# Optimization experiments

Hardware: AMD Instinct MI355X
Metric: run time of the kernel (lower is better)

## Reference

```python
import jax, jax.numpy as jnp
import numpy as np

TOP_K = 2
EPS = 1e-6


def setup_inputs() -> dict:
    key = jax.random.key(0)
    ks = jax.random.split(key, 8)
    B, S, D, E = 4, 2048, 2048, 8
    sd = 1.0 / np.sqrt(D)
    return {
        "x": jax.random.normal(ks[0], (B, S, D), dtype=jnp.float32),
        "Wr": jax.random.normal(ks[1], (D, E), dtype=jnp.float32) * sd,
        "br": jnp.zeros((E,), dtype=jnp.float32),
        "We": jax.random.normal(ks[2], (E, D, D), dtype=jnp.float32) * sd,
        "be": jnp.zeros((E, D), dtype=jnp.float32),
        "Wo": jax.random.normal(ks[3], (D, D), dtype=jnp.float32) * sd,
        "bo": jnp.zeros((D,), dtype=jnp.float32),
        "norm_w": jnp.ones((D,), dtype=jnp.float32),
    }


def reference(x, Wr, br, We, be, Wo, bo, norm_w):
    B, S, D = x.shape
    xf = x.reshape(-1, D)  # [T, D]
    # Router + top-k gating (softmax over the k selected logits, as in source)
    logits = xf @ Wr + br                      # [T, E]
    vals, idx = jax.lax.top_k(logits, TOP_K)   # [T, K]
    gates = jax.nn.softmax(vals, axis=-1)      # [T, K]
    # Expert FFN: Linear -> SiLU (dropout=0 -> identity). Dense over all experts,
    # then gather the top-k outputs per token.
    all_out = jax.nn.silu(jnp.einsum('td,edf->tef', xf, We) + be)  # [T, E, D]
    picked = jnp.take_along_axis(all_out, idx[:, :, None], axis=1)  # [T, K, D]
    combined = jnp.sum(gates[:, :, None] * picked, axis=1)          # [T, D]
    out = combined @ Wo + bo
    y = xf + out
    rms = jnp.sqrt(jnp.mean(y * y, axis=-1, keepdims=True) + EPS)
    return (norm_w * (y / rms)).reshape(B, S, D)
```

## Files before the change

kernel.cpp:

```cpp
#include <hip/hip_runtime.h>
#include <hip/hip_bf16.h>
#include <stdint.h>

typedef __bf16 bf16;
typedef __bf16 bf16x4 __attribute__((ext_vector_type(4)));
typedef __bf16 bf16x8 __attribute__((ext_vector_type(8)));
typedef float floatx4 __attribute__((ext_vector_type(4)));

#define T_TOK 8192
#define DIM 2048
#define NE 8

__device__ inline void gld_lds16(const bf16* g, bf16* l) {
  __builtin_amdgcn_global_load_lds(
      (const __attribute__((address_space(1))) uint32_t*)g,
      (__attribute__((address_space(3))) uint32_t*)l, 16, 0, 0);
}

__global__ __launch_bounds__(256) void transpose_convert(
    const float* __restrict__ in, bf16* __restrict__ out) {
  __shared__ float tile[32][33];
  const int tx = threadIdx.x & 31;
  const int ty = threadIdx.x >> 5;
  const int n0 = blockIdx.x * 32;
  const int k0 = blockIdx.y * 32;
  const size_t base = (size_t)blockIdx.z * DIM * DIM;
  const float* src = in + base;
  bf16* dst = out + base;
#pragma unroll
  for (int i = 0; i < 32; i += 8)
    tile[ty + i][tx] = src[(size_t)(k0 + ty + i) * DIM + n0 + tx];
  __syncthreads();
#pragma unroll
  for (int i = 0; i < 32; i += 8)
    dst[(size_t)(n0 + ty + i) * DIM + k0 + tx] = (bf16)tile[tx][ty + i];
}

__global__ __launch_bounds__(256) void router_kernel(
    const float* __restrict__ x, const float* __restrict__ Wr,
    const float* __restrict__ br, int* __restrict__ cnt,
    int* __restrict__ aid_list, float* __restrict__ gate_list,
    bf16* __restrict__ xb) {
  const int t = blockIdx.x;
  const int tid = threadIdx.x;
  const float* xr = x + (size_t)t * DIM;
  bf16* xbr = xb + (size_t)t * DIM;
  float acc[8];
#pragma unroll
  for (int e = 0; e < 8; ++e) acc[e] = 0.f;
#pragma unroll
  for (int h = 0; h < 2; ++h) {
    const int d0 = tid * 4 + h * 1024;
    float4 xv = *(const float4*)&xr[d0];
    bf16x4 xc;
    xc[0] = (bf16)xv.x; xc[1] = (bf16)xv.y; xc[2] = (bf16)xv.z; xc[3] = (bf16)xv.w;
    *(bf16x4*)&xbr[d0] = xc;
    const float* wp = &Wr[(size_t)d0 * NE];
    float xe[4] = {xv.x, xv.y, xv.z, xv.w};
#pragma unroll
    for (int q = 0; q < 4; ++q) {
      float4 w0 = *(const float4*)&wp[q * 8];
      float4 w1 = *(const float4*)&wp[q * 8 + 4];
      acc[0] += xe[q] * w0.x; acc[1] += xe[q] * w0.y;
      acc[2] += xe[q] * w0.z; acc[3] += xe[q] * w0.w;
      acc[4] += xe[q] * w1.x; acc[5] += xe[q] * w1.y;
      acc[6] += xe[q] * w1.z; acc[7] += xe[q] * w1.w;
    }
  }
#pragma unroll
  for (int e = 0; e < 8; ++e) {
#pragma unroll
    for (int off = 32; off > 0; off >>= 1) acc[e] += __shfl_down(acc[e], off, 64);
  }
  __shared__ float red[4][8];
  const int lane = tid & 63, wid = tid >> 6;
  if (lane == 0) {
#pragma unroll
    for (int e = 0; e < 8; ++e) red[wid][e] = acc[e];
  }
  __syncthreads();
  if (tid == 0) {
    float lg[8];
#pragma unroll
    for (int e = 0; e < 8; ++e)
      lg[e] = red[0][e] + red[1][e] + red[2][e] + red[3][e] + br[e];
    int i0 = 0;
#pragma unroll
    for (int e = 1; e < 8; ++e) if (lg[e] > lg[i0]) i0 = e;
    int i1 = (i0 == 0) ? 1 : 0;
#pragma unroll
    for (int e = 0; e < 8; ++e)
      if (e != i0 && lg[e] > lg[i1]) i1 = e;
    const float g0 = 1.f / (1.f + expf(lg[i1] - lg[i0]));
    const float g1 = 1.f - g0;
    int p0 = atomicAdd(&cnt[i0], 1);
    aid_list[i0 * T_TOK + p0] = t * 2;
    gate_list[i0 * T_TOK + p0] = g0;
    int p1 = atomicAdd(&cnt[i1], 1);
    aid_list[i1 * T_TOK + p1] = t * 2 + 1;
    gate_list[i1 * T_TOK + p1] = g1;
  }
}

__global__ __launch_bounds__(256, 2) void expert_gemm(
    const bf16* __restrict__ xb, const bf16* __restrict__ Wt,
    const float* __restrict__ be, const int* __restrict__ cnt,
    const int* __restrict__ aid_list, const float* __restrict__ gate_list,
    bf16* __restrict__ aout) {
  const int e = blockIdx.z;
  const int ne = cnt[e];
  const int m0 = blockIdx.x * 128;
  if (m0 >= ne) return;
  const int n0 = blockIdx.y * 128;
  const int tid = threadIdx.x;

  __shared__ bf16 As[128][32];
  __shared__ bf16 Bs[128][32];
  __shared__ int aidS[128];
  __shared__ float gateS[128];

  if (tid < 128) {
    const int idx = m0 + tid;
    aidS[tid] = (idx < ne) ? aid_list[e * T_TOK + idx] : 0;
    gateS[tid] = (idx < ne) ? gate_list[e * T_TOK + idx] : 0.f;
  }
  __syncthreads();

  const int kq = (tid & 3) * 8;
  const int row0 = tid >> 2;
  const int row1 = 64 + (tid >> 2);
  const bf16* ap0 = xb + (size_t)(aidS[row0] >> 1) * DIM + kq;
  const bf16* ap1 = xb + (size_t)(aidS[row1] >> 1) * DIM + kq;
  const bf16* wbase = Wt + (size_t)e * DIM * DIM;
  const bf16* bp0 = wbase + (size_t)(n0 + row0) * DIM + kq;
  const bf16* bp1 = wbase + (size_t)(n0 + row1) * DIM + kq;
  bf16* asd0 = &As[0][0] + (size_t)tid * 8;
  bf16* asd1 = &As[0][0] + ((size_t)tid + 256) * 8;
  bf16* bsd0 = &Bs[0][0] + (size_t)tid * 8;
  bf16* bsd1 = &Bs[0][0] + ((size_t)tid + 256) * 8;

  const int lane = tid & 63, wid = tid >> 6;
  const int wr = (wid >> 1) * 64, wc = (wid & 1) * 64;
  const int quad = lane >> 4, l15 = lane & 15;

  floatx4 acc[4][4];
#pragma unroll
  for (int i = 0; i < 4; ++i)
#pragma unroll
    for (int j = 0; j < 4; ++j) acc[i][j] = (floatx4){0.f, 0.f, 0.f, 0.f};

  for (int k0 = 0; k0 < DIM; k0 += 32) {
    gld_lds16(bp0 + k0, bsd0);
    gld_lds16(bp1 + k0, bsd1);
    gld_lds16(ap0 + k0, asd0);
    gld_lds16(ap1 + k0, asd1);
    __syncthreads();

    bf16x8 af[4], bfr[4];
#pragma unroll
    for (int i = 0; i < 4; ++i)
      af[i] = *(const bf16x8*)&As[wr + i * 16 + l15][quad * 8];
#pragma unroll
    for (int j = 0; j < 4; ++j)
      bfr[j] = *(const bf16x8*)&Bs[wc + j * 16 + l15][quad * 8];
#pragma unroll
    for (int i = 0; i < 4; ++i)
#pragma unroll
      for (int j = 0; j < 4; ++j)
        acc[i][j] = __builtin_amdgcn_mfma_f32_16x16x32_bf16(af[i], bfr[j], acc[i][j], 0, 0, 0);
    __syncthreads();
  }

#pragma unroll
  for (int j = 0; j < 4; ++j) {
    const int col = n0 + wc + j * 16 + l15;
    const float bev = be[e * DIM + col];
#pragma unroll
    for (int i = 0; i < 4; ++i) {
#pragma unroll
      for (int r = 0; r < 4; ++r) {
        const int rl = wr + i * 16 + quad * 4 + r;
        if (m0 + rl < ne) {
          float v = acc[i][j][r] + bev;
          v = v / (1.f + __expf(-v));
          v *= gateS[rl];
          aout[(size_t)aidS[rl] * DIM + col] = (bf16)v;
        }
      }
    }
  }
}

__global__ __launch_bounds__(256) void combine_kernel(
    const bf16* __restrict__ aout, bf16* __restrict__ hcomb) {
  const size_t i = ((size_t)blockIdx.x * 256 + threadIdx.x) * 8;
  const size_t row = i >> 11;
  const size_t d = i & 2047;
  const bf16* a0 = aout + (row << 12) + d;
  bf16x8 u0 = *(const bf16x8*)a0;
  bf16x8 u1 = *(const bf16x8*)(a0 + DIM);
  bf16x8 s;
#pragma unroll
  for (int q = 0; q < 8; ++q) s[q] = (bf16)((float)u0[q] + (float)u1[q]);
  *(bf16x8*)&hcomb[i] = s;
}

__global__ __launch_bounds__(256, 2) void proj_gemm(
    const bf16* __restrict__ hcomb, const bf16* __restrict__ Wot,
    const float* __restrict__ bo, const float* __restrict__ x,
    float* __restrict__ y) {
  const int m0 = blockIdx.x * 128;
  const int n0 = blockIdx.y * 128;
  const int tid = threadIdx.x;

  __shared__ bf16 As[128][32];
  __shared__ bf16 Bs[128][32];

  const int kq = (tid & 3) * 8;
  const int row0 = tid >> 2;
  const int row1 = 64 + (tid >> 2);
  const bf16* ap0 = hcomb + (size_t)(m0 + row0) * DIM + kq;
  const bf16* ap1 = hcomb + (size_t)(m0 + row1) * DIM + kq;
  const bf16* bp0 = Wot + (size_t)(n0 + row0) * DIM + kq;
  const bf16* bp1 = Wot + (size_t)(n0 + row1) * DIM + kq;
  bf16* asd0 = &As[0][0] + (size_t)tid * 8;
  bf16* asd1 = &As[0][0] + ((size_t)tid + 256) * 8;
  bf16* bsd0 = &Bs[0][0] + (size_t)tid * 8;
  bf16* bsd1 = &Bs[0][0] + ((size_t)tid + 256) * 8;

  const int lane = tid & 63, wid = tid >> 6;
  const int wr = (wid >> 1) * 64, wc = (wid & 1) * 64;
  const int quad = lane >> 4, l15 = lane & 15;

  floatx4 acc[4][4];
#pragma unroll
  for (int i = 0; i < 4; ++i)
#pragma unroll
    for (int j = 0; j < 4; ++j) acc[i][j] = (floatx4){0.f, 0.f, 0.f, 0.f};

  for (int k0 = 0; k0 < DIM; k0 += 32) {
    gld_lds16(bp0 + k0, bsd0);
    gld_lds16(bp1 + k0, bsd1);
    gld_lds16(ap0 + k0, asd0);
    gld_lds16(ap1 + k0, asd1);
    __syncthreads();

    bf16x8 af[4], bfr[4];
#pragma unroll
    for (int i = 0; i < 4; ++i)
      af[i] = *(const bf16x8*)&As[wr + i * 16 + l15][quad * 8];
#pragma unroll
    for (int j = 0; j < 4; ++j)
      bfr[j] = *(const bf16x8*)&Bs[wc + j * 16 + l15][quad * 8];
#pragma unroll
    for (int i = 0; i < 4; ++i)
#pragma unroll
      for (int j = 0; j < 4; ++j)
        acc[i][j] = __builtin_amdgcn_mfma_f32_16x16x32_bf16(af[i], bfr[j], acc[i][j], 0, 0, 0);
    __syncthreads();
  }

#pragma unroll
  for (int j = 0; j < 4; ++j) {
    const int col = n0 + wc + j * 16 + l15;
    const float bov = bo[col];
#pragma unroll
    for (int i = 0; i < 4; ++i) {
#pragma unroll
      for (int r = 0; r < 4; ++r) {
        const int rl = wr + i * 16 + quad * 4 + r;
        const size_t o = (size_t)(m0 + rl) * DIM + col;
        y[o] = acc[i][j][r] + bov + x[o];
      }
    }
  }
}

__global__ __launch_bounds__(256) void rmsnorm_kernel(
    float* __restrict__ y, const float* __restrict__ w) {
  const int row = blockIdx.x;
  const int tid = threadIdx.x;
  float* yr = y + (size_t)row * DIM;
  float4 v0 = ((const float4*)yr)[tid];
  float4 v1 = ((const float4*)yr)[tid + 256];
  float ss = v0.x * v0.x + v0.y * v0.y + v0.z * v0.z + v0.w * v0.w +
             v1.x * v1.x + v1.y * v1.y + v1.z * v1.z + v1.w * v1.w;
#pragma unroll
  for (int off = 32; off > 0; off >>= 1) ss += __shfl_down(ss, off, 64);
  __shared__ float s4[4];
  const int lane = tid & 63, wid = tid >> 6;
  if (lane == 0) s4[wid] = ss;
  __syncthreads();
  const float tot = s4[0] + s4[1] + s4[2] + s4[3];
  const float r = rsqrtf(tot / (float)DIM + 1e-6f);
  float4 w0 = ((const float4*)w)[tid];
  float4 w1 = ((const float4*)w)[tid + 256];
  float4 o0 = make_float4(v0.x * r * w0.x, v0.y * r * w0.y, v0.z * r * w0.z, v0.w * r * w0.w);
  float4 o1 = make_float4(v1.x * r * w1.x, v1.y * r * w1.y, v1.z * r * w1.z, v1.w * r * w1.w);
  ((float4*)yr)[tid] = o0;
  ((float4*)yr)[tid + 256] = o1;
}

extern "C" void kernel_launch(void* const* d_in, const int* in_sizes, int n_in,
                              void* d_out, int out_size, void* d_ws, size_t ws_size,
                              hipStream_t stream) {
  const float* x  = (const float*)d_in[0];
  const float* Wr = (const float*)d_in[1];
  const float* br = (const float*)d_in[2];
  const float* We = (const float*)d_in[3];
  const float* be = (const float*)d_in[4];
  const float* Wo = (const float*)d_in[5];
  const float* bo = (const float*)d_in[6];
  const float* nw = (const float*)d_in[7];
  float* out = (float*)d_out;

  uint8_t* ws = (uint8_t*)d_ws;
  size_t off = 0;
  auto carve = [&](size_t bytes) -> void* {
    void* p = ws + off;
    off += (bytes + 255) & ~(size_t)255;
    return p;
  };
  int*   cnt       = (int*)carve(NE * sizeof(int));
  int*   aid_list  = (int*)carve((size_t)NE * T_TOK * sizeof(int));
  float* gate_list = (float*)carve((size_t)NE * T_TOK * sizeof(float));
  bf16*  We_t      = (bf16*)carve((size_t)NE * DIM * DIM * sizeof(bf16));
  bf16*  Wo_t      = (bf16*)carve((size_t)DIM * DIM * sizeof(bf16));
  bf16*  aoutb     = (bf16*)carve((size_t)T_TOK * 2 * DIM * sizeof(bf16));
  bf16*  xb        = (bf16*)carve((size_t)T_TOK * DIM * sizeof(bf16));
  bf16*  hcomb     = We_t;
  (void)ws_size; (void)in_sizes; (void)n_in; (void)out_size;

  hipMemsetAsync(cnt, 0, NE * sizeof(int), stream);
  transpose_convert<<<dim3(DIM / 32, DIM / 32, NE), 256, 0, stream>>>(We, We_t);
  transpose_convert<<<dim3(DIM / 32, DIM / 32, 1), 256, 0, stream>>>(Wo, Wo_t);
  router_kernel<<<T_TOK, 256, 0, stream>>>(x, Wr, br, cnt, aid_list, gate_list, xb);
  expert_gemm<<<dim3(T_TOK / 128, DIM / 128, NE), 256, 0, stream>>>(
      xb, We_t, be, cnt, aid_list, gate_list, aoutb);
  combine_kernel<<<(T_TOK * DIM / 8) / 256, 256, 0, stream>>>(aoutb, hcomb);
  proj_gemm<<<dim3(T_TOK / 128, DIM / 128), 256, 0, stream>>>(hcomb, Wo_t, bo, x, out);
  rmsnorm_kernel<<<T_TOK, 256, 0, stream>>>(out, nw);
}
```

Before: 952.8 us.

## Compact expert tile grid and widen GEMM K-tile to 64 with XOR-swizzled LDS

A new single-thread kernel builds a compact list of (expert, row-offset) chunks, so expert_gemm launches only blocks that have work instead of a sparse 64x8 grid where most blocks exit early. Both the expert and projection GEMMs now load 64-wide K tiles per barrier pair, halving the number of synchronizations. An XOR swizzle on the LDS layout is meant to avoid bank conflicts on fragment reads. The cost is an extra tiny serial launch, double the LDS per block (which may lower occupancy), and a fixed MAX_CHUNKS bound.

```diff
diff --git a/kernel.cpp b/kernel.cpp
--- a/kernel.cpp
+++ b/kernel.cpp
@@ -10,6 +10,7 @@
 #define T_TOK 8192
 #define DIM 2048
 #define NE 8
+#define MAX_CHUNKS 136
 
 __device__ inline void gld_lds16(const bf16* g, bf16* l) {
   __builtin_amdgcn_global_load_lds(
@@ -102,20 +103,37 @@
   }
 }
 
+__global__ void build_chunks(const int* __restrict__ cnt, int2* __restrict__ chunks,
+                             int* __restrict__ nchunks) {
+  if (threadIdx.x == 0 && blockIdx.x == 0) {
+    int tot = 0;
+#pragma unroll
+    for (int e = 0; e < NE; ++e) {
+      const int ne = cnt[e];
+      for (int m0 = 0; m0 < ne; m0 += 128) chunks[tot++] = make_int2(e, m0);
+    }
+    *nchunks = tot;
+  }
+}
+
+
 __global__ __launch_bounds__(256, 2) void expert_gemm(
     const bf16* __restrict__ xb, const bf16* __restrict__ Wt,
     const float* __restrict__ be, const int* __restrict__ cnt,
     const int* __restrict__ aid_list, const float* __restrict__ gate_list,
+    const int2* __restrict__ chunks, const int* __restrict__ nchunks,
     bf16* __restrict__ aout) {
-  const int e = blockIdx.z;
+  const int cid = blockIdx.x;
+  if (cid >= *nchunks) return;
+  const int2 ch = chunks[cid];
+  const int e = ch.x;
+  const int m0 = ch.y;
   const int ne = cnt[e];
-  const int m0 = blockIdx.x * 128;
-  if (m0 >= ne) return;
   const int n0 = blockIdx.y * 128;
   const int tid = threadIdx.x;
 
-  __shared__ bf16 As[128][32];
-  __shared__ bf16 Bs[128][32];
+  __shared__ bf16 As[128][64];
+  __shared__ bf16 Bs[128][64];
   __shared__ int aidS[128];
   __shared__ float gateS[128];
 
@@ -126,18 +144,19 @@
   }
   __syncthreads();
 
-  const int kq = (tid & 3) * 8;
-  const int row0 = tid >> 2;
-  const int row1 = 64 + (tid >> 2);
-  const bf16* ap0 = xb + (size_t)(aidS[row0] >> 1) * DIM + kq;
-  const bf16* ap1 = xb + (size_t)(aidS[row1] >> 1) * DIM + kq;
+  const int r0 = tid >> 3;
+  const int kq = (((tid & 7) ^ (r0 & 7))) * 8;
   const bf16* wbase = Wt + (size_t)e * DIM * DIM;
-  const bf16* bp0 = wbase + (size_t)(n0 + row0) * DIM + kq;
-  const bf16* bp1 = wbase + (size_t)(n0 + row1) * DIM + kq;
-  bf16* asd0 = &As[0][0] + (size_t)tid * 8;
-  bf16* asd1 = &As[0][0] + ((size_t)tid + 256) * 8;
-  bf16* bsd0 = &Bs[0][0] + (size_t)tid * 8;
-  bf16* bsd1 = &Bs[0][0] + ((size_t)tid + 256) * 8;
+  const bf16* ap[4];
+  const bf16* bp[4];
+#pragma unroll
+  for (int h = 0; h < 4; ++h) {
+    const int r = r0 + 32 * h;
+    ap[h] = xb + (size_t)(aidS[r] >> 1) * DIM + kq;
+    bp[h] = wbase + (size_t)(n0 + r) * DIM + kq;
+  }
+  bf16* const asF = &As[0][0];
+  bf16* const bsF = &Bs[0][0];
 
   const int lane = tid & 63, wid = tid >> 6;
   const int wr = (wid >> 1) * 64, wc = (wid & 1) * 64;
@@ -149,25 +168,40 @@
 #pragma unroll
     for (int j = 0; j < 4; ++j) acc[i][j] = (floatx4){0.f, 0.f, 0.f, 0.f};
 
-  for (int k0 = 0; k0 < DIM; k0 += 32) {
-    gld_lds16(bp0 + k0, bsd0);
-    gld_lds16(bp1 + k0, bsd1);
-    gld_lds16(ap0 + k0, asd0);
-    gld_lds16(ap1 + k0, asd1);
+  int aoff[2][4], boff[2][4];
+#pragma unroll
+  for (int s = 0; s < 2; ++s) {
+    const int kb = s * 4 + quad;
+#pragma unroll
+    for (int i = 0; i < 4; ++i) {
+      const int mi = wr + i * 16 + l15;
+      aoff[s][i] = mi * 64 + ((kb ^ (mi & 7)) * 8);
+      const int nj = wc + i * 16 + l15;
+      boff[s][i] = nj * 64 + ((kb ^ (nj & 7)) * 8);
+    }
+  }
+
+  for (int k0 = 0; k0 < DIM; k0 += 64) {
+#pragma unroll
+    for (int h = 0; h < 4; ++h) {
+      gld_lds16(bp[h] + k0, bsF + ((size_t)tid + 256 * h) * 8);
+      gld_lds16(ap[h] + k0, asF + ((size_t)tid + 256 * h) * 8);
+    }
     __syncthreads();
 
-    bf16x8 af[4], bfr[4];
-#pragma unroll
-    for (int i = 0; i < 4; ++i)
-      af[i] = *(const bf16x8*)&As[wr + i * 16 + l15][quad * 8];
-#pragma unroll
-    for (int j = 0; j < 4; ++j)
-      bfr[j] = *(const bf16x8*)&Bs[wc + j * 16 + l15][quad * 8];
-#pragma unroll
-    for (int i = 0; i < 4; ++i)
-#pragma unroll
-      for (int j = 0; j < 4; ++j)
-        acc[i][j] = __builtin_amdgcn_mfma_f32_16x16x32_bf16(af[i], bfr[j], acc[i][j], 0, 0, 0);
+#pragma unroll
+    for (int s = 0; s < 2; ++s) {
+      bf16x8 af[4], bfr[4];
+#pragma unroll
+      for (int i = 0; i < 4; ++i) af[i] = *(const bf16x8*)&asF[aoff[s][i]];
+#pragma unroll
+      for (int j = 0; j < 4; ++j) bfr[j] = *(const bf16x8*)&bsF[boff[s][j]];
+#pragma unroll
+      for (int i = 0; i < 4; ++i)
+#pragma unroll
+        for (int j = 0; j < 4; ++j)
+          acc[i][j] = __builtin_amdgcn_mfma_f32_16x16x32_bf16(af[i], bfr[j], acc[i][j], 0, 0, 0);
+    }
     __syncthreads();
   }
 
@@ -213,20 +247,21 @@
   const int n0 = blockIdx.y * 128;
   const int tid = threadIdx.x;
 
-  __shared__ bf16 As[128][32];
-  __shared__ bf16 Bs[128][32];
-
-  const int kq = (tid & 3) * 8;
-  const int row0 = tid >> 2;
-  const int row1 = 64 + (tid >> 2);
-  const bf16* ap0 = hcomb + (size_t)(m0 + row0) * DIM + kq;
-  const bf16* ap1 = hcomb + (size_t)(m0 + row1) * DIM + kq;
-  const bf16* bp0 = Wot + (size_t)(n0 + row0) * DIM + kq;
-  const bf16* bp1 = Wot + (size_t)(n0 + row1) * DIM + kq;
-  bf16* asd0 = &As[0][0] + (size_t)tid * 8;
-  bf16* asd1 = &As[0][0] + ((size_t)tid + 256) * 8;
-  bf16* bsd0 = &Bs[0][0] + (size_t)tid * 8;
-  bf16* bsd1 = &Bs[0][0] + ((size_t)tid + 256) * 8;
+  __shared__ bf16 As[128][64];
+  __shared__ bf16 Bs[128][64];
+
+  const int r0 = tid >> 3;
+  const int kq = (((tid & 7) ^ (r0 & 7))) * 8;
+  const bf16* ap[4];
+  const bf16* bp[4];
+#pragma unroll
+  for (int h = 0; h < 4; ++h) {
+    const int r = r0 + 32 * h;
+    ap[h] = hcomb + (size_t)(m0 + r) * DIM + kq;
+    bp[h] = Wot + (size_t)(n0 + r) * DIM + kq;
+  }
+  bf16* const asF = &As[0][0];
+  bf16* const bsF = &Bs[0][0];
 
   const int lane = tid & 63, wid = tid >> 6;
   const int wr = (wid >> 1) * 64, wc = (wid & 1) * 64;
@@ -238,25 +273,40 @@
 #pragma unroll
     for (int j = 0; j < 4; ++j) acc[i][j] = (floatx4){0.f, 0.f, 0.f, 0.f};
 
-  for (int k0 = 0; k0 < DIM; k0 += 32) {
-    gld_lds16(bp0 + k0, bsd0);
-    gld_lds16(bp1 + k0, bsd1);
-    gld_lds16(ap0 + k0, asd0);
-    gld_lds16(ap1 + k0, asd1);
+  int aoff[2][4], boff[2][4];
+#pragma unroll
+  for (int s = 0; s < 2; ++s) {
+    const int kb = s * 4 + quad;
+#pragma unroll
+    for (int i = 0; i < 4; ++i) {
+      const int mi = wr + i * 16 + l15;
+      aoff[s][i] = mi * 64 + ((kb ^ (mi & 7)) * 8);
+      const int nj = wc + i * 16 + l15;
+      boff[s][i] = nj * 64 + ((kb ^ (nj & 7)) * 8);
+    }
+  }
+
+  for (int k0 = 0; k0 < DIM; k0 += 64) {
+#pragma unroll
+    for (int h = 0; h < 4; ++h) {
+      gld_lds16(bp[h] + k0, bsF + ((size_t)tid + 256 * h) * 8);
+      gld_lds16(ap[h] + k0, asF + ((size_t)tid + 256 * h) * 8);
+    }
     __syncthreads();
 
-    bf16x8 af[4], bfr[4];
-#pragma unroll
-    for (int i = 0; i < 4; ++i)
-      af[i] = *(const bf16x8*)&As[wr + i * 16 + l15][quad * 8];
-#pragma unroll
-    for (int j = 0; j < 4; ++j)
-      bfr[j] = *(const bf16x8*)&Bs[wc + j * 16 + l15][quad * 8];
-#pragma unroll
-    for (int i = 0; i < 4; ++i)
-#pragma unroll
-      for (int j = 0; j < 4; ++j)
-        acc[i][j] = __builtin_amdgcn_mfma_f32_16x16x32_bf16(af[i], bfr[j], acc[i][j], 0, 0, 0);
+#pragma unroll
+    for (int s = 0; s < 2; ++s) {
+      bf16x8 af[4], bfr[4];
+#pragma unroll
+      for (int i = 0; i < 4; ++i) af[i] = *(const bf16x8*)&asF[aoff[s][i]];
+#pragma unroll
+      for (int j = 0; j < 4; ++j) bfr[j] = *(const bf16x8*)&bsF[boff[s][j]];
+#pragma unroll
+      for (int i = 0; i < 4; ++i)
+#pragma unroll
+        for (int j = 0; j < 4; ++j)
+          acc[i][j] = __builtin_amdgcn_mfma_f32_16x16x32_bf16(af[i], bfr[j], acc[i][j], 0, 0, 0);
+    }
     __syncthreads();
   }
 
@@ -324,6 +374,8 @@
   int*   cnt       = (int*)carve(NE * sizeof(int));
   int*   aid_list  = (int*)carve((size_t)NE * T_TOK * sizeof(int));
   float* gate_list = (float*)carve((size_t)NE * T_TOK * sizeof(float));
+  int2*  chunks    = (int2*)carve(MAX_CHUNKS * sizeof(int2));
+  int*   nchunks   = (int*)carve(sizeof(int));
   bf16*  We_t      = (bf16*)carve((size_t)NE * DIM * DIM * sizeof(bf16));
   bf16*  Wo_t      = (bf16*)carve((size_t)DIM * DIM * sizeof(bf16));
   bf16*  aoutb     = (bf16*)carve((size_t)T_TOK * 2 * DIM * sizeof(bf16));
@@ -335,8 +387,9 @@
   transpose_convert<<<dim3(DIM / 32, DIM / 32, NE), 256, 0, stream>>>(We, We_t);
   transpose_convert<<<dim3(DIM / 32, DIM / 32, 1), 256, 0, stream>>>(Wo, Wo_t);
   router_kernel<<<T_TOK, 256, 0, stream>>>(x, Wr, br, cnt, aid_list, gate_list, xb);
-  expert_gemm<<<dim3(T_TOK / 128, DIM / 128, NE), 256, 0, stream>>>(
-      xb, We_t, be, cnt, aid_list, gate_list, aoutb);
+  build_chunks<<<1, 64, 0, stream>>>(cnt, chunks, nchunks);
+  expert_gemm<<<dim3(MAX_CHUNKS, DIM / 128), 256, 0, stream>>>(
+      xb, We_t, be, cnt, aid_list, gate_list, chunks, nchunks, aoutb);
   combine_kernel<<<(T_TOK * DIM / 8) / 256, 256, 0, stream>>>(aoutb, hcomb);
   proj_gemm<<<dim3(T_TOK / 128, DIM / 128), 256, 0, stream>>>(hcomb, Wo_t, bo, x, out);
   rmsnorm_kernel<<<T_TOK, 256, 0, stream>>>(out, nw);
```

New measurement: 838.9 us. -12.0%, faster.
